# Performance work log

Hardware: AMD Instinct MI355X
Metric: run time of the kernel (lower is better)

The kernel has to match this reference:

```python
import jax, jax.numpy as jnp
import numpy as np

B, I, H = 16384, 1024, 1024

def setup_inputs() -> dict:
    key = jax.random.key(0)
    ks = jax.random.split(key, 6)
    s_i = 1.0 / np.sqrt(I)
    s_h = 1.0 / np.sqrt(H)
    return {
        "incoming": jax.random.normal(ks[0], (B, I), dtype=jnp.float32),
        "old_h": jax.random.normal(ks[1], (B, H), dtype=jnp.float32),
        "old_c": jax.random.normal(ks[2], (B, H), dtype=jnp.float32),
        # 4 gates stacked: order [i, f, g, o] matching the torch ModuleList indices 0..3
        "Wi": jax.random.uniform(ks[3], (4, H, I), minval=-s_i, maxval=s_i, dtype=jnp.float32),
        "bi": jax.random.uniform(ks[4], (4, H), minval=-s_i, maxval=s_i, dtype=jnp.float32),
        "Wh": jax.random.uniform(ks[5], (4, H, H), minval=-s_h, maxval=s_h, dtype=jnp.float32),
    }

def reference(incoming, old_h, old_c, Wi, bi, Wh):
    # two batched GEMMs producing all 4 gate pre-activations: [4, B, H]
    gates = (jnp.einsum('bi,ghi->gbh', incoming, Wi)
             + jnp.einsum('bh,gkh->gbk', old_h, Wh)
             + bi[:, None, :])
    i = jax.nn.sigmoid(gates[0])
    f = jax.nn.sigmoid(gates[1])
    g = jnp.tanh(gates[2])
    o = jax.nn.sigmoid(gates[3])
    new_c = f * old_c + i * g
    new_h = o * jnp.tanh(new_c)
    return (new_h, (new_h, new_c))
```

## Files before the change

kernel.cpp:

```cpp
#include <hip/hip_runtime.h>
#include <hip/hip_bf16.h>
#include <math.h>

#define B_SZ 16384
#define H_SZ 1024
#define K_SZ 2048
#define OUT_PLANE ((size_t)B_SZ * H_SZ)

#define BM 128
#define BH 32
#define BK 64

typedef __bf16 bf16;
typedef __attribute__((ext_vector_type(8))) __bf16 bf16x8;
typedef __attribute__((ext_vector_type(4))) float floatx4;

__device__ __forceinline__ void gload_lds16(const bf16* g, bf16* l) {
    __builtin_amdgcn_global_load_lds(
        (const __attribute__((address_space(1))) void*)g,
        (__attribute__((address_space(3))) void*)l, 16, 0, 0);
}

__device__ __forceinline__ float sigmoidf_fast(float x) {
    return 1.f / (1.f + __expf(-x));
}

__global__ void cvt_x(const float* __restrict__ inc, const float* __restrict__ oh,
                      bf16* __restrict__ X) {
    size_t t  = (size_t)blockIdx.x * blockDim.x + threadIdx.x;
    size_t e0 = t * 8;
    size_t b  = e0 >> 11;
    int    k  = (int)(e0 & 2047);
    const float* src = (k < 1024) ? (inc + b * 1024 + k)
                                  : (oh  + b * 1024 + (k - 1024));
    floatx4 f0 = *(const floatx4*)src;
    floatx4 f1 = *(const floatx4*)(src + 4);
    bf16x8 o;
    o[0]=(bf16)f0[0]; o[1]=(bf16)f0[1]; o[2]=(bf16)f0[2]; o[3]=(bf16)f0[3];
    o[4]=(bf16)f1[0]; o[5]=(bf16)f1[1]; o[6]=(bf16)f1[2]; o[7]=(bf16)f1[3];
    *(bf16x8*)(X + e0) = o;
}

__global__ void cvt_w(const float* __restrict__ Wi, const float* __restrict__ Wh,
                      bf16* __restrict__ W) {
    size_t t  = (size_t)blockIdx.x * blockDim.x + threadIdx.x;
    size_t e0 = t * 8;
    size_t n  = e0 >> 11;
    int    k  = (int)(e0 & 2047);
    const float* src = (k < 1024) ? (Wi + n * 1024 + k)
                                  : (Wh + n * 1024 + (k - 1024));
    floatx4 f0 = *(const floatx4*)src;
    floatx4 f1 = *(const floatx4*)(src + 4);
    bf16x8 o;
    o[0]=(bf16)f0[0]; o[1]=(bf16)f0[1]; o[2]=(bf16)f0[2]; o[3]=(bf16)f0[3];
    o[4]=(bf16)f1[0]; o[5]=(bf16)f1[1]; o[6]=(bf16)f1[2]; o[7]=(bf16)f1[3];
    *(bf16x8*)(W + e0) = o;
}

__global__ __launch_bounds__(256, 2) void lstm_gemm(
    const bf16* __restrict__ X, const bf16* __restrict__ W,
    const float* __restrict__ bi, const float* __restrict__ oldc,
    float* __restrict__ out) {
    __shared__ bf16 As[BM * BK];
    __shared__ bf16 Bs[128 * BK];

    const int tid  = threadIdx.x;
    const int lane = tid & 63;
    const int wv   = tid >> 6;
    const int h0   = blockIdx.x * BH;
    const int brow0 = blockIdx.y * BM;

    floatx4 acc[4][2][2];
    #pragma unroll
    for (int g = 0; g < 4; ++g)
        #pragma unroll
        for (int n = 0; n < 2; ++n)
            #pragma unroll
            for (int m = 0; m < 2; ++m) {
                floatx4 z = {0.f, 0.f, 0.f, 0.f};
                acc[g][n][m] = z;
            }

    const int lrow = lane >> 3;
    const int lcol = (lane & 7) * 8;

    const bf16* xg = X + (size_t)(brow0 + wv * 8 + lrow) * K_SZ + lcol;

    for (int kt = 0; kt < K_SZ; kt += BK) {
        #pragma unroll
        for (int r = 0; r < 4; ++r) {
            gload_lds16(xg + (size_t)(r * 32) * K_SZ + kt,
                        As + (r * 32 + wv * 8) * BK);
        }
        #pragma unroll
        for (int r = 0; r < 4; ++r) {
            int rb   = r * 32 + wv * 8 + lrow;
            int wrow = ((rb >> 5) << 10) + h0 + (rb & 31);
            gload_lds16(W + (size_t)wrow * K_SZ + kt + lcol,
                        Bs + (r * 32 + wv * 8) * BK);
        }
        __syncthreads();

        #pragma unroll
        for (int kk = 0; kk < BK; kk += 32) {
            const int arow = wv * 32 + (lane & 15);
            const int koff = kk + ((lane >> 4) << 3);
            bf16x8 a0 = *(const bf16x8*)(As + (size_t)(arow     ) * BK + koff);
            bf16x8 a1 = *(const bf16x8*)(As + (size_t)(arow + 16) * BK + koff);
            #pragma unroll
            for (int g = 0; g < 4; ++g) {
                #pragma unroll
                for (int n = 0; n < 2; ++n) {
                    bf16x8 bfr = *(const bf16x8*)(
                        Bs + (size_t)(g * 32 + n * 16 + (lane & 15)) * BK + koff);
                    acc[g][n][0] = __builtin_amdgcn_mfma_f32_16x16x32_bf16(
                        a0, bfr, acc[g][n][0], 0, 0, 0);
                    acc[g][n][1] = __builtin_amdgcn_mfma_f32_16x16x32_bf16(
                        a1, bfr, acc[g][n][1], 0, 0, 0);
                }
            }
        }
        __syncthreads();
    }

    float* outh  = out;
    float* outh2 = out + OUT_PLANE;
    float* outc  = out + 2 * OUT_PLANE;
    #pragma unroll
    for (int n = 0; n < 2; ++n) {
        const int h  = h0 + n * 16 + (lane & 15);
        const float b_i = bi[h];
        const float b_f = bi[H_SZ + h];
        const float b_g = bi[2 * H_SZ + h];
        const float b_o = bi[3 * H_SZ + h];
        #pragma unroll
        for (int m = 0; m < 2; ++m) {
            const int brow = brow0 + wv * 32 + m * 16 + ((lane >> 4) << 2);
            #pragma unroll
            for (int r = 0; r < 4; ++r) {
                const size_t idx = (size_t)(brow + r) * H_SZ + h;
                float gi = acc[0][n][m][r] + b_i;
                float gf = acc[1][n][m][r] + b_f;
                float gg = acc[2][n][m][r] + b_g;
                float go = acc[3][n][m][r] + b_o;
                float iv = sigmoidf_fast(gi);
                float fv = sigmoidf_fast(gf);
                float gv = tanhf(gg);
                float ov = sigmoidf_fast(go);
                float c  = fv * oldc[idx] + iv * gv;
                float hv = ov * tanhf(c);
                outh[idx]  = hv;
                outh2[idx] = hv;
                outc[idx]  = c;
            }
        }
    }
}

__global__ void lstm_fallback(const float* __restrict__ X, const float* __restrict__ Ho,
                              const float* __restrict__ Co, const float* __restrict__ Wi,
                              const float* __restrict__ bi, const float* __restrict__ Wh,
                              float* __restrict__ out) {
    int b = blockIdx.x;
    __shared__ float xs[1024], hs[1024];
    for (int k = threadIdx.x; k < 1024; k += blockDim.x) {
        xs[k] = X[(size_t)b * 1024 + k];
        hs[k] = Ho[(size_t)b * 1024 + k];
    }
    __syncthreads();
    for (int h = threadIdx.x; h < 1024; h += blockDim.x) {
        float g[4];
        for (int gg = 0; gg < 4; ++gg) {
            const float* wi = Wi + ((size_t)gg * 1024 + h) * 1024;
            const float* wh = Wh + ((size_t)gg * 1024 + h) * 1024;
            float acc = bi[gg * 1024 + h];
            for (int k = 0; k < 1024; ++k) acc += xs[k] * wi[k] + hs[k] * wh[k];
            g[gg] = acc;
        }
        float iv = sigmoidf_fast(g[0]);
        float fv = sigmoidf_fast(g[1]);
        float gv = tanhf(g[2]);
        float ov = sigmoidf_fast(g[3]);
        float c  = fv * Co[(size_t)b * 1024 + h] + iv * gv;
        float hv = ov * tanhf(c);
        size_t idx = (size_t)b * 1024 + h;
        out[idx] = hv;
        out[OUT_PLANE + idx] = hv;
        out[2 * OUT_PLANE + idx] = c;
    }
}

extern "C" void kernel_launch(void* const* d_in, const int* in_sizes, int n_in,
                              void* d_out, int out_size, void* d_ws, size_t ws_size,
                              hipStream_t stream) {
    const float* incoming = (const float*)d_in[0];
    const float* old_h    = (const float*)d_in[1];
    const float* old_c    = (const float*)d_in[2];
    const float* Wi       = (const float*)d_in[3];
    const float* bi       = (const float*)d_in[4];
    const float* Wh       = (const float*)d_in[5];
    float* out = (float*)d_out;

    const size_t nX = (size_t)B_SZ * K_SZ;
    const size_t nW = (size_t)4 * H_SZ * K_SZ;
    if (ws_size < (nX + nW) * sizeof(bf16)) {
        lstm_fallback<<<B_SZ, 256, 0, stream>>>(incoming, old_h, old_c, Wi, bi, Wh, out);
        return;
    }
    bf16* X = (bf16*)d_ws;
    bf16* W = X + nX;

    cvt_x<<<(int)(nX / 8 / 256), 256, 0, stream>>>(incoming, old_h, X);
    cvt_w<<<(int)(nW / 8 / 256), 256, 0, stream>>>(Wi, Wh, W);

    dim3 grid(H_SZ / BH, B_SZ / BM);
    lstm_gemm<<<grid, 256, 0, stream>>>(X, W, bi, old_c, out);
}
```

Before: 710.8 us.

## XOR-swizzle LDS tiles, merge conversion kernels, fast tanh, raise occupancy bound

Applies an XOR swizzle to the 16-byte chunk index of the A and B LDS tiles so that MFMA operand reads avoid bank conflicts. It also merges the two fp32-to-bf16 conversion kernels into one launch, replaces tanhf with an exp-based approximation in the epilogue, and raises the launch-bounds occupancy hint from 2 to 4 blocks per CU. The higher occupancy hint may limit registers and cause spills, since each thread holds 64 accumulator floats. The fast tanh trades a little accuracy for cheaper transcendental math.

```diff
diff --git a/kernel.cpp b/kernel.cpp
--- a/kernel.cpp
+++ b/kernel.cpp
@@ -24,40 +24,39 @@
 __device__ __forceinline__ float sigmoidf_fast(float x) {
     return 1.f / (1.f + __expf(-x));
 }
-
-__global__ void cvt_x(const float* __restrict__ inc, const float* __restrict__ oh,
-                      bf16* __restrict__ X) {
+__device__ __forceinline__ float tanhf_fast(float x) {
+    return 2.f / (1.f + __expf(-2.f * x)) - 1.f;
+}
+
+__global__ void cvt_all(const float* __restrict__ inc, const float* __restrict__ oh,
+                        const float* __restrict__ Wi, const float* __restrict__ Wh,
+                        bf16* __restrict__ X, bf16* __restrict__ W) {
+    const size_t nX = (size_t)B_SZ * K_SZ;
     size_t t  = (size_t)blockIdx.x * blockDim.x + threadIdx.x;
     size_t e0 = t * 8;
-    size_t b  = e0 >> 11;
-    int    k  = (int)(e0 & 2047);
-    const float* src = (k < 1024) ? (inc + b * 1024 + k)
-                                  : (oh  + b * 1024 + (k - 1024));
+    const float* src;
+    bf16* dst;
+    if (e0 < nX) {
+        size_t b = e0 >> 11;
+        int    k = (int)(e0 & 2047);
+        src = (k < 1024) ? (inc + b * 1024 + k) : (oh + b * 1024 + (k - 1024));
+        dst = X + e0;
+    } else {
+        size_t e = e0 - nX;
+        size_t n = e >> 11;
+        int    k = (int)(e & 2047);
+        src = (k < 1024) ? (Wi + n * 1024 + k) : (Wh + n * 1024 + (k - 1024));
+        dst = W + e;
+    }
     floatx4 f0 = *(const floatx4*)src;
     floatx4 f1 = *(const floatx4*)(src + 4);
     bf16x8 o;
     o[0]=(bf16)f0[0]; o[1]=(bf16)f0[1]; o[2]=(bf16)f0[2]; o[3]=(bf16)f0[3];
     o[4]=(bf16)f1[0]; o[5]=(bf16)f1[1]; o[6]=(bf16)f1[2]; o[7]=(bf16)f1[3];
-    *(bf16x8*)(X + e0) = o;
-}
-
-__global__ void cvt_w(const float* __restrict__ Wi, const float* __restrict__ Wh,
-                      bf16* __restrict__ W) {
-    size_t t  = (size_t)blockIdx.x * blockDim.x + threadIdx.x;
-    size_t e0 = t * 8;
-    size_t n  = e0 >> 11;
-    int    k  = (int)(e0 & 2047);
-    const float* src = (k < 1024) ? (Wi + n * 1024 + k)
-                                  : (Wh + n * 1024 + (k - 1024));
-    floatx4 f0 = *(const floatx4*)src;
-    floatx4 f1 = *(const floatx4*)(src + 4);
-    bf16x8 o;
-    o[0]=(bf16)f0[0]; o[1]=(bf16)f0[1]; o[2]=(bf16)f0[2]; o[3]=(bf16)f0[3];
-    o[4]=(bf16)f1[0]; o[5]=(bf16)f1[1]; o[6]=(bf16)f1[2]; o[7]=(bf16)f1[3];
-    *(bf16x8*)(W + e0) = o;
-}
-
-__global__ __launch_bounds__(256, 2) void lstm_gemm(
+    *(bf16x8*)dst = o;
+}
+
+__global__ __launch_bounds__(256, 4) void lstm_gemm(
     const bf16* __restrict__ X, const bf16* __restrict__ W,
     const float* __restrict__ bi, const float* __restrict__ oldc,
     float* __restrict__ out) {
@@ -82,7 +81,7 @@
             }
 
     const int lrow = lane >> 3;
-    const int lcol = (lane & 7) * 8;
+    const int lcol = (((lane & 7) ^ lrow) * 8);
 
     const bf16* xg = X + (size_t)(brow0 + wv * 8 + lrow) * K_SZ + lcol;
 
@@ -103,16 +102,21 @@
 
         #pragma unroll
         for (int kk = 0; kk < BK; kk += 32) {
-            const int arow = wv * 32 + (lane & 15);
-            const int koff = kk + ((lane >> 4) << 3);
-            bf16x8 a0 = *(const bf16x8*)(As + (size_t)(arow     ) * BK + koff);
-            bf16x8 a1 = *(const bf16x8*)(As + (size_t)(arow + 16) * BK + koff);
+            const int q    = lane >> 4;
+            const int cidx = (kk >> 3) + q;
+            const int arow0 = wv * 32 + (lane & 15);
+            const int arow1 = arow0 + 16;
+            bf16x8 a0 = *(const bf16x8*)(
+                As + (size_t)arow0 * BK + ((cidx ^ (arow0 & 7)) * 8));
+            bf16x8 a1 = *(const bf16x8*)(
+                As + (size_t)arow1 * BK + ((cidx ^ (arow1 & 7)) * 8));
             #pragma unroll
             for (int g = 0; g < 4; ++g) {
                 #pragma unroll
                 for (int n = 0; n < 2; ++n) {
+                    const int brow = g * 32 + n * 16 + (lane & 15);
                     bf16x8 bfr = *(const bf16x8*)(
-                        Bs + (size_t)(g * 32 + n * 16 + (lane & 15)) * BK + koff);
+                        Bs + (size_t)brow * BK + ((cidx ^ (brow & 7)) * 8));
                     acc[g][n][0] = __builtin_amdgcn_mfma_f32_16x16x32_bf16(
                         a0, bfr, acc[g][n][0], 0, 0, 0);
                     acc[g][n][1] = __builtin_amdgcn_mfma_f32_16x16x32_bf16(
@@ -145,10 +149,10 @@
                 float go = acc[3][n][m][r] + b_o;
                 float iv = sigmoidf_fast(gi);
                 float fv = sigmoidf_fast(gf);
-                float gv = tanhf(gg);
+                float gv = tanhf_fast(gg);
                 float ov = sigmoidf_fast(go);
                 float c  = fv * oldc[idx] + iv * gv;
-                float hv = ov * tanhf(c);
+                float hv = ov * tanhf_fast(c);
                 outh[idx]  = hv;
                 outh2[idx] = hv;
                 outc[idx]  = c;
@@ -174,15 +178,15 @@
             const float* wi = Wi + ((size_t)gg * 1024 + h) * 1024;
             const float* wh = Wh + ((size_t)gg * 1024 + h) * 1024;
             float acc = bi[gg * 1024 + h];
-            for (int k = 0; k < 1024; ++k) acc += xs[k] * wi[k] + hs[k] * wh[k];
+        for (int k = 0; k < 1024; ++k) acc += xs[k] * wi[k] + hs[k] * wh[k];
             g[gg] = acc;
         }
         float iv = sigmoidf_fast(g[0]);
         float fv = sigmoidf_fast(g[1]);
-        float gv = tanhf(g[2]);
+        float gv = tanhf_fast(g[2]);
         float ov = sigmoidf_fast(g[3]);
         float c  = fv * Co[(size_t)b * 1024 + h] + iv * gv;
-        float hv = ov * tanhf(c);
+        float hv = ov * tanhf_fast(c);
         size_t idx = (size_t)b * 1024 + h;
         out[idx] = hv;
         out[OUT_PLANE + idx] = hv;
@@ -210,8 +214,8 @@
     bf16* X = (bf16*)d_ws;
     bf16* W = X + nX;
 
-    cvt_x<<<(int)(nX / 8 / 256), 256, 0, stream>>>(incoming, old_h, X);
-    cvt_w<<<(int)(nW / 8 / 256), 256, 0, stream>>>(Wi, Wh, W);
+    const int cvt_blocks = (int)((nX + nW) / 8 / 256);
+    cvt_all<<<cvt_blocks, 256, 0, stream>>>(incoming, old_h, Wi, Wh, X, W);
 
     dim3 grid(H_SZ / BH, B_SZ / BM);
     lstm_gemm<<<grid, 256, 0, stream>>>(X, W, bi, old_c, out);
```

New measurement: 613.7 us. 1.16x faster.
